# Kernel tuning notes

Measured on AMD Instinct MI355X. Metric: run time of the kernel, lower is better.

The kernel has to match this reference:

```python
import jax, jax.numpy as jnp
import numpy as np


def setup_inputs() -> dict:
    key = jax.random.key(0)
    kq, kk, kv = jax.random.split(key, 3)
    B, H, S, D = 2, 16, 2048, 128
    return {
        "query_states": jax.random.normal(kq, (B, H, S, D), dtype=jnp.float32),
        "key_states": jax.random.normal(kk, (B, H, S, D), dtype=jnp.float32),
        "value_states": jax.random.normal(kv, (B, H, S, D), dtype=jnp.float32),
    }


def reference(query_states, key_states, value_states):
    # Faithful translation of CoreAttention.forward with attention_mask=None,
    # attention_dropout=0.0 (default, and dropout with p=0 is identity).
    B, H, Sq, D = query_states.shape
    Skv = key_states.shape[-2]
    scale = 1.0 / jnp.sqrt(jnp.asarray(D, dtype=query_states.dtype))
    # [B,H,Sq,Skv] score matrix (the module materializes this explicitly)
    attn_weights = jnp.einsum("bhqd,bhkd->bhqk", query_states, key_states) * scale
    # internal causal mask: triu(ones, diagonal=1) positions -> dtype min
    causal = jnp.triu(jnp.ones((Sq, Skv), dtype=bool), k=1)
    mask_value = jnp.finfo(attn_weights.dtype).min
    attn_weights = jnp.where(causal[None, None], mask_value, attn_weights)
    # torch does softmax in float64 then casts back; numerically stable fp32
    # softmax is equivalent to working precision here (jax x64 disabled).
    attn_weights = jax.nn.softmax(attn_weights, axis=-1).astype(query_states.dtype)
    attn_output = jnp.einsum("bhqk,bhkd->bhqd", attn_weights, value_states)
    return attn_output
```

## Files before the change

kernel.cpp:

```cpp
#include <hip/hip_runtime.h>
#include <hip/hip_bf16.h>
#include <stdint.h>

typedef __bf16  bf16x8 __attribute__((ext_vector_type(8)));
typedef __bf16  bf16x4 __attribute__((ext_vector_type(4)));
typedef float   f32x4  __attribute__((ext_vector_type(4)));
typedef uint32_t u32x4 __attribute__((ext_vector_type(4)));

#define SLEN  2048
#define DHEAD 128
#define QBLK  64
#define KVBLK 32
#define NQT   (SLEN / QBLK)
#define THR2  11.5415603f

__device__ __forceinline__ uint32_t cvt_pk(float lo, float hi2) {
    uint32_t u;
    asm("v_cvt_pk_bf16_f32 %0, %1, %2" : "=v"(u) : "v"(lo), "v"(hi2));
    return u;
}

__device__ __forceinline__ float exp2fast(float x) {
    return __builtin_amdgcn_exp2f(x);
}

__global__ __launch_bounds__(256, 3) void attn_fwd(
    const float* __restrict__ Q, const float* __restrict__ K,
    const float* __restrict__ V, float* __restrict__ O)
{
    const int bh = blockIdx.x;
    const int qt = (NQT - 1) - blockIdx.y;
    const int tid  = threadIdx.x;
    const int w    = tid >> 6;
    const int lane = tid & 63;
    const int r    = lane & 15;
    const int g    = lane >> 4;

    const size_t head_off = (size_t)bh * SLEN * DHEAD;
    const float* Qh = Q + head_off;
    const float* Kh = K + head_off;
    const float* Vh = V + head_off;
    float*       Oh = O + head_off;

    const int q0w = qt * QBLK + w * 16;

    __shared__ __bf16 K_sh [2][KVBLK * DHEAD];
    __shared__ __bf16 Vt_sh[2][DHEAD * 40];

    const float scale = 0.08838834764831845f * 1.4426950408889634f;

    bf16x8 qfrag[4];
    {
        const float4* qp = reinterpret_cast<const float4*>(
            Qh + (size_t)(q0w + r) * DHEAD + g * 8);
        #pragma unroll
        for (int kb = 0; kb < 4; ++kb) {
            float4 a = qp[kb*8 + 0];
            float4 b = qp[kb*8 + 1];
            a.x*=scale; a.y*=scale; a.z*=scale; a.w*=scale;
            b.x*=scale; b.y*=scale; b.z*=scale; b.w*=scale;
            bf16x8 f;
            f[0]=(__bf16)a.x; f[1]=(__bf16)a.y; f[2]=(__bf16)a.z; f[3]=(__bf16)a.w;
            f[4]=(__bf16)b.x; f[5]=(__bf16)b.y; f[6]=(__bf16)b.z; f[7]=(__bf16)b.w;
            qfrag[kb] = f;
        }
    }

    float4 kreg[4], vreg[4];
    const int c4  = tid & 31;
    const int kvq = tid >> 5;

    auto issue_loads = [&](int kv0) {
        #pragma unroll
        for (int it = 0; it < 4; ++it) {
            const int row = (it * 256 + tid) >> 5;
            kreg[it] = *reinterpret_cast<const float4*>(
                Kh + (size_t)(kv0 + row) * DHEAD + c4 * 4);
        }
        #pragma unroll
        for (int kr = 0; kr < 4; ++kr)
            vreg[kr] = *reinterpret_cast<const float4*>(
                Vh + (size_t)(kv0 + kvq * 4 + kr) * DHEAD + c4 * 4);
    };

    auto write_tiles = [&](int buf) {
        char* Kb  = reinterpret_cast<char*>(K_sh[buf]);
        char* Vtb = reinterpret_cast<char*>(Vt_sh[buf]);
        #pragma unroll
        for (int it = 0; it < 4; ++it) {
            const int row = (it * 256 + tid) >> 5;
            bf16x4 k4;
            k4[0]=(__bf16)kreg[it].x; k4[1]=(__bf16)kreg[it].y;
            k4[2]=(__bf16)kreg[it].z; k4[3]=(__bf16)kreg[it].w;
            *reinterpret_cast<bf16x4*>(
                Kb + row * 256 + ((c4 * 8) ^ ((row & 15) << 4))) = k4;
        }
        #pragma unroll
        for (int j = 0; j < 4; ++j) {
            const int d = c4 * 4 + j;
            bf16x4 v4;
            #pragma unroll
            for (int kr = 0; kr < 4; ++kr)
                v4[kr] = (__bf16)((&vreg[kr].x)[j]);
            *reinterpret_cast<bf16x4*>(
                Vtb + d * 80 + ((kvq ^ ((d >> 2) & 6)) * 8)) = v4;
        }
    };

    const f32x4 vzero = {0.f, 0.f, 0.f, 0.f};
    f32x4 acc_o[8];
    #pragma unroll
    for (int i = 0; i < 8; ++i) acc_o[i] = vzero;
    float m_run = -1e30f, l_run = 0.f;

    const int n_iter = 2 * qt + 2;
    const int my_max = (q0w + 15) >> 5;

    auto do_qk = [&](f32x4* st, int t, int kb_buf) {
        char* Kb = reinterpret_cast<char*>(K_sh[kb_buf]);
        const bool a1 = (t * KVBLK + 16 <= q0w + 15);
        __builtin_amdgcn_s_setprio(1);
        #pragma unroll
        for (int tt = 0; tt < 2; ++tt) {
            st[tt] = vzero;
            if (tt == 1 && !a1) break;
            const int row = tt * 16 + r;
            #pragma unroll
            for (int kb = 0; kb < 4; ++kb) {
                bf16x8 kf = *reinterpret_cast<const bf16x8*>(
                    Kb + row * 256 + ((kb*64 + g*16) ^ ((row & 15) << 4)));
                st[tt] = __builtin_amdgcn_mfma_f32_16x16x32_bf16(
                    kf, qfrag[kb], st[tt], 0, 0, 0);
            }
        }
        __builtin_amdgcn_s_setprio(0);
    };

    auto process = [&](f32x4* st, int t, int vt_buf) {
        const int kv0 = t * KVBLK;
        char* Vtb = reinterpret_cast<char*>(Vt_sh[vt_buf]);
        const bool alive1 = (kv0 + 16 <= q0w + 15);

        const int q = q0w + r;
        float pmax = -1e30f;
        #pragma unroll
        for (int tt = 0; tt < 2; ++tt) {
            if (tt == 1 && !alive1) break;
            if (kv0 + tt*16 + 15 > q0w) {
                #pragma unroll
                for (int j = 0; j < 4; ++j)
                    if (kv0 + tt*16 + 4*g + j > q) st[tt][j] = -1e30f;
            }
            #pragma unroll
            for (int j = 0; j < 4; ++j) pmax = fmaxf(pmax, st[tt][j]);
        }
        pmax = fmaxf(pmax, __shfl_xor(pmax, 16));
        pmax = fmaxf(pmax, __shfl_xor(pmax, 32));

        if (__any(pmax > m_run + THR2)) {
            const float m_new = fmaxf(m_run, pmax);
            const float corr  = exp2fast(m_run - m_new);
            l_run *= corr; m_run = m_new;
            #pragma unroll
            for (int reg = 0; reg < 4; ++reg) {
                const float cr = __shfl(corr, 4*g + reg);
                #pragma unroll
                for (int dt = 0; dt < 8; ++dt) acc_o[dt][reg] *= cr;
            }
        }

        float rowsum = 0.f;
        #pragma unroll
        for (int tt = 0; tt < 2; ++tt) {
            if (tt == 1 && !alive1) break;
            #pragma unroll
            for (int j = 0; j < 4; ++j) {
                const float p = exp2fast(st[tt][j] - m_run);
                st[tt][j] = p;
                rowsum += p;
            }
        }
        rowsum += __shfl_xor(rowsum, 16);
        rowsum += __shfl_xor(rowsum, 32);
        l_run += rowsum;

        const uint32_t p00 = cvt_pk(st[0][0], st[0][1]);
        const uint32_t p01 = cvt_pk(st[0][2], st[0][3]);
        const uint32_t p10 = alive1 ? cvt_pk(st[1][0], st[1][1]) : 0u;
        const uint32_t p11 = alive1 ? cvt_pk(st[1][2], st[1][3]) : 0u;
        const int sA = r + ((2 * (g & 1)) << 4);
        const int sB = r + ((2 * (g & 1) + 1) << 4);
        u32x4 words;
        {
            const uint32_t lo0 = (uint32_t)__shfl((int)p00, sA);
            const uint32_t hi0 = (uint32_t)__shfl((int)p10, sA);
            const uint32_t lo1 = (uint32_t)__shfl((int)p01, sA);
            const uint32_t hi1 = (uint32_t)__shfl((int)p11, sA);
            const uint32_t lo2 = (uint32_t)__shfl((int)p00, sB);
            const uint32_t hi2 = (uint32_t)__shfl((int)p10, sB);
            const uint32_t lo3 = (uint32_t)__shfl((int)p01, sB);
            const uint32_t hi3 = (uint32_t)__shfl((int)p11, sB);
            words[0] = (g & 2) ? hi0 : lo0;
            words[1] = (g & 2) ? hi1 : lo1;
            words[2] = (g & 2) ? hi2 : lo2;
            words[3] = (g & 2) ? hi3 : lo3;
        }
        const bf16x8 pa = __builtin_bit_cast(bf16x8, words);

        __builtin_amdgcn_s_setprio(1);
        #pragma unroll
        for (int dt = 0; dt < 8; ++dt) {
            const int d = dt * 16 + r;
            bf16x8 vf = *reinterpret_cast<const bf16x8*>(
                Vtb + d * 80 + (((2*g) ^ ((d >> 2) & 6)) * 8));
            acc_o[dt] = __builtin_amdgcn_mfma_f32_16x16x32_bf16(
                pa, vf, acc_o[dt], 0, 0, 0);
        }
        __builtin_amdgcn_s_setprio(0);
    };

    issue_loads(0);
    write_tiles(0);
    __syncthreads();
    issue_loads(KVBLK);
    f32x4 stA[2] = {vzero, vzero};
    f32x4 stB[2] = {vzero, vzero};
    do_qk(stA, 0, 0);
    write_tiles(1);

    for (int i = 0; i < n_iter; i += 2) {
        __syncthreads();
        if (i + 2 < n_iter) issue_loads((i + 2) * KVBLK);
        if (i + 1 <= my_max) do_qk(stB, i + 1, 1);
        if (i     <= my_max) process(stA, i, 0);
        __syncthreads();
        if (i + 2 < n_iter) write_tiles(0);

        __syncthreads();
        if (i + 3 < n_iter) issue_loads((i + 3) * KVBLK);
        if (i + 2 <= my_max) do_qk(stA, i + 2, 0);
        if (i + 1 <= my_max) process(stB, i + 1, 1);
        __syncthreads();
        if (i + 3 < n_iter) write_tiles(1);
    }

    const float inv = 1.0f / l_run;
    #pragma unroll
    for (int reg = 0; reg < 4; ++reg) {
        const float iv = __shfl(inv, 4*g + reg);
        float* orow = Oh + (size_t)(q0w + 4*g + reg) * DHEAD + r;
        #pragma unroll
        for (int dt = 0; dt < 8; ++dt)
            orow[dt * 16] = acc_o[dt][reg] * iv;
    }
}

extern "C" void kernel_launch(void* const* d_in, const int* in_sizes, int n_in,
                              void* d_out, int out_size, void* d_ws, size_t ws_size,
                              hipStream_t stream) {
    const float* Q = (const float*)d_in[0];
    const float* K = (const float*)d_in[1];
    const float* V = (const float*)d_in[2];
    float* O = (float*)d_out;
    dim3 grid(32 , NQT);
    attn_fwd<<<grid, 256, 0, stream>>>(Q, K, V, O);
}
```

Measured before the change: 91.86 us.

## Pre-pack K/V to swizzled bf16 tiles and stream via global_load_lds

Adds a pre-pass kernel that converts K and V to bf16 once per call into a workspace. K is laid out as swizzled tiles and V as transposed swizzled tiles. The attention kernel then copies each tile straight into LDS with global_load_lds, replacing the per-block fp32 loads, register conversions and transposes. The main loop becomes a simpler single-stage double buffer, and launch bounds rise to 4 blocks per CU. This removes redundant conversion work repeated across the 32 q-tiles. In exchange it costs an extra launch plus a workspace write and read, and loses the QK/softmax software pipelining of the previous loop.

```diff
diff --git a/kernel.cpp b/kernel.cpp
--- a/kernel.cpp
+++ b/kernel.cpp
@@ -7,11 +7,10 @@
 typedef float   f32x4  __attribute__((ext_vector_type(4)));
 typedef uint32_t u32x4 __attribute__((ext_vector_type(4)));
 
-#define SLEN  2048
-#define DHEAD 128
-#define QBLK  64
+#define S     2048
+#define D     128
 #define KVBLK 32
-#define NQT   (SLEN / QBLK)
+#define NQT   32
 #define THR2  11.5415603f
 
 __device__ __forceinline__ uint32_t cvt_pk(float lo, float hi2) {
@@ -19,14 +18,73 @@
     asm("v_cvt_pk_bf16_f32 %0, %1, %2" : "=v"(u) : "v"(lo), "v"(hi2));
     return u;
 }
-
 __device__ __forceinline__ float exp2fast(float x) {
     return __builtin_amdgcn_exp2f(x);
 }
-
-__global__ __launch_bounds__(256, 3) void attn_fwd(
-    const float* __restrict__ Q, const float* __restrict__ K,
-    const float* __restrict__ V, float* __restrict__ O)
+__device__ __forceinline__ void gl2lds16(const void* g, void* l) {
+    __builtin_amdgcn_global_load_lds(
+        (const __attribute__((address_space(1))) void*)g,
+        (__attribute__((address_space(3))) void*)l, 16, 0, 0);
+}
+
+__global__ __launch_bounds__(256) void pack_kv(
+    const float* __restrict__ K, const float* __restrict__ V,
+    __bf16* __restrict__ Kp, __bf16* __restrict__ Vp)
+{
+    const int bh = blockIdx.x, t = blockIdx.y;
+    const int tid = threadIdx.x;
+    const int kv0 = t * KVBLK;
+
+    {
+        const float* src = K + ((size_t)bh * S + kv0) * D;
+        char* dst = (char*)Kp + ((size_t)(bh * 64 + t)) * 8192;
+        #pragma unroll
+        for (int cc = 0; cc < 2; ++cc) {
+            const int c = cc * 256 + tid;
+            const int row = c >> 4, col16 = c & 15;
+            const float4 a = *reinterpret_cast<const float4*>(src + row * D + col16 * 8);
+            const float4 b = *reinterpret_cast<const float4*>(src + row * D + col16 * 8 + 4);
+            bf16x8 o;
+            o[0]=(__bf16)a.x; o[1]=(__bf16)a.y; o[2]=(__bf16)a.z; o[3]=(__bf16)a.w;
+            o[4]=(__bf16)b.x; o[5]=(__bf16)b.y; o[6]=(__bf16)b.z; o[7]=(__bf16)b.w;
+            *reinterpret_cast<bf16x8*>(
+                dst + row * 256 + ((col16 * 16) ^ ((row & 15) << 4))) = o;
+        }
+    }
+
+    __shared__ __bf16 lds[32][136];
+    {
+        const float* src = V + ((size_t)bh * S + kv0) * D;
+        #pragma unroll
+        for (int it = 0; it < 4; ++it) {
+            const int id = it * 256 + tid;
+            const int row = id >> 5, c4 = id & 31;
+            float4 v = *reinterpret_cast<const float4*>(src + row * D + c4 * 4);
+            bf16x4 b4;
+            b4[0]=(__bf16)v.x; b4[1]=(__bf16)v.y; b4[2]=(__bf16)v.z; b4[3]=(__bf16)v.w;
+            *reinterpret_cast<bf16x4*>(&lds[row][c4 * 4]) = b4;
+        }
+    }
+    __syncthreads();
+    {
+        char* dst = (char*)Vp + ((size_t)(bh * 64 + t)) * 8192;
+        #pragma unroll
+        for (int cc = 0; cc < 2; ++cc) {
+            const int c = cc * 256 + tid;
+            const int d = c >> 2, c8 = c & 3;
+            bf16x8 o;
+            #pragma unroll
+            for (int k = 0; k < 8; ++k) o[k] = lds[c8 * 8 + k][d];
+            const int addr = (d >> 1) * 128 +
+                ((((d & 1) << 6) + c8 * 16) ^ (((d >> 1) & 3) << 4));
+            *reinterpret_cast<bf16x8*>(dst + addr) = o;
+        }
+    }
+}
+
+__global__ __launch_bounds__(256, 4) void attn_fwd(
+    const float* __restrict__ Q, const __bf16* __restrict__ Kp,
+    const __bf16* __restrict__ Vp, float* __restrict__ O)
 {
     const int bh = blockIdx.x;
     const int qt = (NQT - 1) - blockIdx.y;
@@ -36,23 +94,22 @@
     const int r    = lane & 15;
     const int g    = lane >> 4;
 
-    const size_t head_off = (size_t)bh * SLEN * DHEAD;
-    const float* Qh = Q + head_off;
-    const float* Kh = K + head_off;
-    const float* Vh = V + head_off;
-    float*       Oh = O + head_off;
-
-    const int q0w = qt * QBLK + w * 16;
-
-    __shared__ __bf16 K_sh [2][KVBLK * DHEAD];
-    __shared__ __bf16 Vt_sh[2][DHEAD * 40];
+    const float* Qh = Q + (size_t)bh * S * D;
+    float*       Oh = O + (size_t)bh * S * D;
+    const char*  Kbase = (const char*)Kp + (size_t)bh * 64 * 8192;
+    const char*  Vbase = (const char*)Vp + (size_t)bh * 64 * 8192;
+
+    const int q0w = qt * 64 + w * 16;
+
+    __shared__ __align__(16) __bf16 K_sh[2][KVBLK * D];
+    __shared__ __align__(16) __bf16 V_sh[2][D * KVBLK];
 
     const float scale = 0.08838834764831845f * 1.4426950408889634f;
 
     bf16x8 qfrag[4];
     {
         const float4* qp = reinterpret_cast<const float4*>(
-            Qh + (size_t)(q0w + r) * DHEAD + g * 8);
+            Qh + (size_t)(q0w + r) * D + g * 8);
         #pragma unroll
         for (int kb = 0; kb < 4; ++kb) {
             float4 a = qp[kb*8 + 0];
@@ -66,45 +123,15 @@
         }
     }
 
-    float4 kreg[4], vreg[4];
-    const int c4  = tid & 31;
-    const int kvq = tid >> 5;
-
-    auto issue_loads = [&](int kv0) {
-        #pragma unroll
-        for (int it = 0; it < 4; ++it) {
-            const int row = (it * 256 + tid) >> 5;
-            kreg[it] = *reinterpret_cast<const float4*>(
-                Kh + (size_t)(kv0 + row) * DHEAD + c4 * 4);
-        }
-        #pragma unroll
-        for (int kr = 0; kr < 4; ++kr)
-            vreg[kr] = *reinterpret_cast<const float4*>(
-                Vh + (size_t)(kv0 + kvq * 4 + kr) * DHEAD + c4 * 4);
-    };
-
-    auto write_tiles = [&](int buf) {
-        char* Kb  = reinterpret_cast<char*>(K_sh[buf]);
-        char* Vtb = reinterpret_cast<char*>(Vt_sh[buf]);
-        #pragma unroll
-        for (int it = 0; it < 4; ++it) {
-            const int row = (it * 256 + tid) >> 5;
-            bf16x4 k4;
-            k4[0]=(__bf16)kreg[it].x; k4[1]=(__bf16)kreg[it].y;
-            k4[2]=(__bf16)kreg[it].z; k4[3]=(__bf16)kreg[it].w;
-            *reinterpret_cast<bf16x4*>(
-                Kb + row * 256 + ((c4 * 8) ^ ((row & 15) << 4))) = k4;
-        }
-        #pragma unroll
-        for (int j = 0; j < 4; ++j) {
-            const int d = c4 * 4 + j;
-            bf16x4 v4;
-            #pragma unroll
-            for (int kr = 0; kr < 4; ++kr)
-                v4[kr] = (__bf16)((&vreg[kr].x)[j]);
-            *reinterpret_cast<bf16x4*>(
-                Vtb + d * 80 + ((kvq ^ ((d >> 2) & 6)) * 8)) = v4;
-        }
+    auto STAGE = [&](int buf, int t) {
+        const char* ks = Kbase + (size_t)t * 8192 + w * 1024 + lane * 16;
+        const char* vs = Vbase + (size_t)t * 8192 + w * 1024 + lane * 16;
+        char* kd = (char*)(&K_sh[buf][0]) + w * 1024;
+        char* vd = (char*)(&V_sh[buf][0]) + w * 1024;
+        gl2lds16(ks,        kd);
+        gl2lds16(ks + 4096, kd + 4096);
+        gl2lds16(vs,        vd);
+        gl2lds16(vs + 4096, vd + 4096);
     };
 
     const f32x4 vzero = {0.f, 0.f, 0.f, 0.f};
@@ -116,139 +143,123 @@
     const int n_iter = 2 * qt + 2;
     const int my_max = (q0w + 15) >> 5;
 
-    auto do_qk = [&](f32x4* st, int t, int kb_buf) {
-        char* Kb = reinterpret_cast<char*>(K_sh[kb_buf]);
-        const bool a1 = (t * KVBLK + 16 <= q0w + 15);
-        __builtin_amdgcn_s_setprio(1);
-        #pragma unroll
-        for (int tt = 0; tt < 2; ++tt) {
-            st[tt] = vzero;
-            if (tt == 1 && !a1) break;
-            const int row = tt * 16 + r;
-            #pragma unroll
-            for (int kb = 0; kb < 4; ++kb) {
-                bf16x8 kf = *reinterpret_cast<const bf16x8*>(
-                    Kb + row * 256 + ((kb*64 + g*16) ^ ((row & 15) << 4)));
-                st[tt] = __builtin_amdgcn_mfma_f32_16x16x32_bf16(
-                    kf, qfrag[kb], st[tt], 0, 0, 0);
-            }
-        }
-        __builtin_amdgcn_s_setprio(0);
-    };
-
-    auto process = [&](f32x4* st, int t, int vt_buf) {
-        const int kv0 = t * KVBLK;
-        char* Vtb = reinterpret_cast<char*>(Vt_sh[vt_buf]);
-        const bool alive1 = (kv0 + 16 <= q0w + 15);
-
-        const int q = q0w + r;
-        float pmax = -1e30f;
-        #pragma unroll
-        for (int tt = 0; tt < 2; ++tt) {
-            if (tt == 1 && !alive1) break;
-            if (kv0 + tt*16 + 15 > q0w) {
-                #pragma unroll
-                for (int j = 0; j < 4; ++j)
-                    if (kv0 + tt*16 + 4*g + j > q) st[tt][j] = -1e30f;
-            }
-            #pragma unroll
-            for (int j = 0; j < 4; ++j) pmax = fmaxf(pmax, st[tt][j]);
-        }
-        pmax = fmaxf(pmax, __shfl_xor(pmax, 16));
-        pmax = fmaxf(pmax, __shfl_xor(pmax, 32));
-
-        if (__any(pmax > m_run + THR2)) {
-            const float m_new = fmaxf(m_run, pmax);
-            const float corr  = exp2fast(m_run - m_new);
-            l_run *= corr; m_run = m_new;
-            #pragma unroll
-            for (int reg = 0; reg < 4; ++reg) {
-                const float cr = __shfl(corr, 4*g + reg);
-                #pragma unroll
-                for (int dt = 0; dt < 8; ++dt) acc_o[dt][reg] *= cr;
-            }
-        }
-
-        float rowsum = 0.f;
-        #pragma unroll
-        for (int tt = 0; tt < 2; ++tt) {
-            if (tt == 1 && !alive1) break;
-            #pragma unroll
-            for (int j = 0; j < 4; ++j) {
-                const float p = exp2fast(st[tt][j] - m_run);
-                st[tt][j] = p;
-                rowsum += p;
-            }
-        }
-        rowsum += __shfl_xor(rowsum, 16);
-        rowsum += __shfl_xor(rowsum, 32);
-        l_run += rowsum;
-
-        const uint32_t p00 = cvt_pk(st[0][0], st[0][1]);
-        const uint32_t p01 = cvt_pk(st[0][2], st[0][3]);
-        const uint32_t p10 = alive1 ? cvt_pk(st[1][0], st[1][1]) : 0u;
-        const uint32_t p11 = alive1 ? cvt_pk(st[1][2], st[1][3]) : 0u;
-        const int sA = r + ((2 * (g & 1)) << 4);
-        const int sB = r + ((2 * (g & 1) + 1) << 4);
-        u32x4 words;
-        {
-            const uint32_t lo0 = (uint32_t)__shfl((int)p00, sA);
-            const uint32_t hi0 = (uint32_t)__shfl((int)p10, sA);
-            const uint32_t lo1 = (uint32_t)__shfl((int)p01, sA);
-            const uint32_t hi1 = (uint32_t)__shfl((int)p11, sA);
-            const uint32_t lo2 = (uint32_t)__shfl((int)p00, sB);
-            const uint32_t hi2 = (uint32_t)__shfl((int)p10, sB);
-            const uint32_t lo3 = (uint32_t)__shfl((int)p01, sB);
-            const uint32_t hi3 = (uint32_t)__shfl((int)p11, sB);
-            words[0] = (g & 2) ? hi0 : lo0;
-            words[1] = (g & 2) ? hi1 : lo1;
-            words[2] = (g & 2) ? hi2 : lo2;
-            words[3] = (g & 2) ? hi3 : lo3;
-        }
-        const bf16x8 pa = __builtin_bit_cast(bf16x8, words);
-
-        __builtin_amdgcn_s_setprio(1);
-        #pragma unroll
-        for (int dt = 0; dt < 8; ++dt) {
-            const int d = dt * 16 + r;
-            bf16x8 vf = *reinterpret_cast<const bf16x8*>(
-                Vtb + d * 80 + (((2*g) ^ ((d >> 2) & 6)) * 8));
-            acc_o[dt] = __builtin_amdgcn_mfma_f32_16x16x32_bf16(
-                pa, vf, acc_o[dt], 0, 0, 0);
-        }
-        __builtin_amdgcn_s_setprio(0);
-    };
-
-    issue_loads(0);
-    write_tiles(0);
+    STAGE(0, 0);
     __syncthreads();
-    issue_loads(KVBLK);
-    f32x4 stA[2] = {vzero, vzero};
-    f32x4 stB[2] = {vzero, vzero};
-    do_qk(stA, 0, 0);
-    write_tiles(1);
-
-    for (int i = 0; i < n_iter; i += 2) {
+    int cur = 0;
+
+    for (int t = 0; t < n_iter; ++t) {
+        if (t + 1 < n_iter) STAGE(cur ^ 1, t + 1);
+
+        if (t <= my_max) {
+            const int kv0 = t * KVBLK;
+            char* Kb = reinterpret_cast<char*>(&K_sh[cur][0]);
+            char* Vb = reinterpret_cast<char*>(&V_sh[cur][0]);
+            const bool alive1 = (kv0 + 16 <= q0w + 15);
+
+            f32x4 st[2] = {vzero, vzero};
+            __builtin_amdgcn_s_setprio(1);
+            #pragma unroll
+            for (int tt = 0; tt < 2; ++tt) {
+                if (tt == 1 && !alive1) break;
+                const int row = tt * 16 + r;
+                #pragma unroll
+                for (int kb = 0; kb < 4; ++kb) {
+                    bf16x8 kf = *reinterpret_cast<const bf16x8*>(
+                        Kb + row * 256 + ((kb*64 + g*16) ^ ((row & 15) << 4)));
+                    st[tt] = __builtin_amdgcn_mfma_f32_16x16x32_bf16(
+                        kf, qfrag[kb], st[tt], 0, 0, 0);
+                }
+            }
+            __builtin_amdgcn_s_setprio(0);
+
+            const int q = q0w + r;
+            float pmax = -1e30f;
+            #pragma unroll
+            for (int tt = 0; tt < 2; ++tt) {
+                if (tt == 1 && !alive1) break;
+                if (kv0 + tt*16 + 15 > q0w) {
+                    #pragma unroll
+                    for (int jj = 0; jj < 4; ++jj)
+                        if (kv0 + tt*16 + 4*g + jj > q) st[tt][jj] = -1e30f;
+                }
+                #pragma unroll
+                for (int jj = 0; jj < 4; ++jj) pmax = fmaxf(pmax, st[tt][jj]);
+            }
+            pmax = fmaxf(pmax, __shfl_xor(pmax, 16));
+            pmax = fmaxf(pmax, __shfl_xor(pmax, 32));
+
+            if (__any(pmax > m_run + THR2)) {
+                const float m_new = fmaxf(m_run, pmax);
+                const float corr  = exp2fast(m_run - m_new);
+                l_run *= corr; m_run = m_new;
+                #pragma unroll
+                for (int reg = 0; reg < 4; ++reg) {
+                    const float cr = __shfl(corr, 4*g + reg);
+                    #pragma unroll
+                    for (int dt = 0; dt < 8; ++dt) acc_o[dt][reg] *= cr;
+                }
+            }
+
+            float rowsum = 0.f;
+            #pragma unroll
+            for (int tt = 0; tt < 2; ++tt) {
+                if (tt == 1 && !alive1) break;
+                #pragma unroll
+                for (int jj = 0; jj < 4; ++jj) {
+                    const float p = exp2fast(st[tt][jj] - m_run);
+                    st[tt][jj] = p;
+                    rowsum += p;
+                }
+            }
+            rowsum += __shfl_xor(rowsum, 16);
+            rowsum += __shfl_xor(rowsum, 32);
+            l_run += rowsum;
+
+            const uint32_t p00 = cvt_pk(st[0][0], st[0][1]);
+            const uint32_t p01 = cvt_pk(st[0][2], st[0][3]);
+            const uint32_t p10 = alive1 ? cvt_pk(st[1][0], st[1][1]) : 0u;
+            const uint32_t p11 = alive1 ? cvt_pk(st[1][2], st[1][3]) : 0u;
+            const int sA = r + ((2 * (g & 1)) << 4);
+            const int sB = r + ((2 * (g & 1) + 1) << 4);
+            u32x4 words;
+            {
+                const uint32_t lo0 = (uint32_t)__shfl((int)p00, sA);
+                const uint32_t hi0 = (uint32_t)__shfl((int)p10, sA);
+                const uint32_t lo1 = (uint32_t)__shfl((int)p01, sA);
+                const uint32_t hi1 = (uint32_t)__shfl((int)p11, sA);
+                const uint32_t lo2 = (uint32_t)__shfl((int)p00, sB);
+                const uint32_t hi2 = (uint32_t)__shfl((int)p10, sB);
+                const uint32_t lo3 = (uint32_t)__shfl((int)p01, sB);
+                const uint32_t hi3 = (uint32_t)__shfl((int)p11, sB);
+                words[0] = (g & 2) ? hi0 : lo0;
+                words[1] = (g & 2) ? hi1 : lo1;
+                words[2] = (g & 2) ? hi2 : lo2;
+                words[3] = (g & 2) ? hi3 : lo3;
+            }
+            const bf16x8 pa = __builtin_bit_cast(bf16x8, words);
+
+            __builtin_amdgcn_s_setprio(1);
+            #pragma unroll
+            for (int dt = 0; dt < 8; ++dt) {
+                const int d = dt * 16 + r;
+                const int byte = (d >> 1) * 128 +
+                    ((((d & 1) << 6) + (g << 4)) ^ (((d >> 1) & 3) << 4));
+                bf16x8 vf = *reinterpret_cast<const bf16x8*>(Vb + byte);
+                acc_o[dt] = __builtin_amdgcn_mfma_f32_16x16x32_bf16(
+                    pa, vf, acc_o[dt], 0, 0, 0);
+            }
+            __builtin_amdgcn_s_setprio(0);
+        }
+
         __syncthreads();
-        if (i + 2 < n_iter) issue_loads((i + 2) * KVBLK);
-        if (i + 1 <= my_max) do_qk(stB, i + 1, 1);
-        if (i     <= my_max) process(stA, i, 0);
-        __syncthreads();
-        if (i + 2 < n_iter) write_tiles(0);
-
-        __syncthreads();
-        if (i + 3 < n_iter) issue_loads((i + 3) * KVBLK);
-        if (i + 2 <= my_max) do_qk(stA, i + 2, 0);
-        if (i + 1 <= my_max) process(stB, i + 1, 1);
-        __syncthreads();
-        if (i + 3 < n_iter) write_tiles(1);
+        cur ^= 1;
     }
 
     const float inv = 1.0f / l_run;
     #pragma unroll
     for (int reg = 0; reg < 4; ++reg) {
         const float iv = __shfl(inv, 4*g + reg);
-        float* orow = Oh + (size_t)(q0w + 4*g + reg) * DHEAD + r;
+        float* orow = Oh + (size_t)(q0w + 4*g + reg) * D + r;
         #pragma unroll
         for (int dt = 0; dt < 8; ++dt)
             orow[dt * 16] = acc_o[dt][reg] * iv;
@@ -262,6 +273,10 @@
     const float* K = (const float*)d_in[1];
     const float* V = (const float*)d_in[2];
     float* O = (float*)d_out;
-    dim3 grid(32 , NQT);
-    attn_fwd<<<grid, 256, 0, stream>>>(Q, K, V, O);
-}
+
+    __bf16* Kp = (__bf16*)d_ws;
+    __bf16* Vp = Kp + (size_t)32 * S * D;
+
+    pack_kv<<<dim3(32, 64), 256, 0, stream>>>(K, V, Kp, Vp);
+    attn_fwd<<<dim3(32, NQT), 256, 0, stream>>>(Q, Kp, Vp, O);
+}
```

Result: slower. 104.2 us (+13.5%).
